# Kernel optimization log

Measured on AMD Instinct MI355X. Metric: run time of the kernel, lower is better.

Reference implementation:

```python
import jax, jax.numpy as jnp
import numpy as np

N_NODES = 50000
N_EDGES = 800000
F_IN = 128
F_OUT = 64
ALPHA = 0.2  # LeakyReLU negative slope


def setup_inputs() -> dict:
    key = jax.random.key(0)
    k1, k2, k3, k4, k5, k6 = jax.random.split(key, 6)
    inp = jax.random.normal(k1, (N_NODES, F_IN), dtype=jnp.float32)
    W = jax.random.normal(k2, (F_IN, F_OUT), dtype=jnp.float32) * 0.05
    a = jax.random.normal(k3, (1, 2 * F_OUT), dtype=jnp.float32) * 0.05
    adj_vals = jax.random.uniform(k4, (N_EDGES,), dtype=jnp.float32)
    src = jax.random.randint(k5, (N_EDGES,), 0, N_NODES)
    dst = jax.random.randint(k6, (N_EDGES,), 0, N_NODES)
    edge_index = jnp.stack([src, dst], axis=0).astype(jnp.int64)
    return {"input": inp, "W": W, "a": a, "adj_vals": adj_vals, "edge_index": edge_index}


def reference(input, W, a, adj_vals, edge_index):
    N = input.shape[0]
    src, dst = edge_index[0], edge_index[1]
    # h = input @ W  (dropout is identity in eval mode)
    h = input @ W  # (N, F_OUT)
    # a.mm(edge_h) with edge_h = [h[src]; h[dst]] decomposes into two per-node dots
    a_src, a_dst = a[0, :F_OUT], a[0, F_OUT:]
    score_src = h @ a_src  # (N,)
    score_dst = h @ a_dst  # (N,)
    scores = score_src[src] + score_dst[dst]  # (E,)
    edge_e = jnp.exp(-jax.nn.leaky_relu(scores, ALPHA)) * adj_vals  # (E,)
    # sparse spmm: row-sum normalizer and weighted aggregation over neighbors
    e_rowsum = jax.ops.segment_sum(edge_e, src, num_segments=N)  # (N,)
    h_prime = jax.ops.segment_sum(edge_e[:, None] * h[dst], src, num_segments=N)  # (N, F_OUT)
    h_prime = h_prime / e_rowsum[:, None]
    return jax.nn.elu(h_prime)  # concat=True
```

## Files before the change

### kernel.cpp

```cpp
#include <hip/hip_runtime.h>
#include <math.h>

#define N_NODES 50000
#define N_EDGES 800000
#define F_IN    128
#define F_OUT   64
#define ALPHA   0.2f

#define NP      50176
#define NB      196

__global__ __launch_bounds__(256) void k_gemm_scores(
    const float* __restrict__ in, const float* __restrict__ W,
    const float* __restrict__ a, float* __restrict__ h,
    float* __restrict__ ssrc, float* __restrict__ sdst) {
  __shared__ float Ws[F_IN][F_OUT];
  __shared__ float As[64][68];
  __shared__ float al[2 * F_OUT];

  const int tid  = threadIdx.x;
  const int row0 = blockIdx.x * 64;

  {
    const float4* Wg = reinterpret_cast<const float4*>(W);
    float4* Wl = reinterpret_cast<float4*>(&Ws[0][0]);
    #pragma unroll
    for (int i = 0; i < 8; ++i) Wl[tid + i * 256] = Wg[tid + i * 256];
  }
  if (tid < 2 * F_OUT) al[tid] = a[tid];

  const int rg = tid >> 4;
  const int cg = tid & 15;
  const int sr = tid >> 2;
  const int sq = tid & 3;
  int grow = row0 + sr; if (grow >= N_NODES) grow = N_NODES - 1;

  float acc[4][4] = {{0.f}};

  for (int kc = 0; kc < 2; ++kc) {
    if (kc) __syncthreads();
    #pragma unroll
    for (int i = 0; i < 4; ++i) {
      const int slot = sq + 4 * i;
      const float4 v = *reinterpret_cast<const float4*>(
          in + (size_t)grow * F_IN + kc * 64 + slot * 4);
      As[slot * 4 + 0][sr] = v.x;
      As[slot * 4 + 1][sr] = v.y;
      As[slot * 4 + 2][sr] = v.z;
      As[slot * 4 + 3][sr] = v.w;
    }
    __syncthreads();

    #pragma unroll 8
    for (int kk = 0; kk < 64; ++kk) {
      const float4 av = *reinterpret_cast<const float4*>(&As[kk][rg * 4]);
      const float4 bv = *reinterpret_cast<const float4*>(&Ws[kc * 64 + kk][cg * 4]);
      acc[0][0] = fmaf(av.x, bv.x, acc[0][0]);
      acc[0][1] = fmaf(av.x, bv.y, acc[0][1]);
      acc[0][2] = fmaf(av.x, bv.z, acc[0][2]);
      acc[0][3] = fmaf(av.x, bv.w, acc[0][3]);
      acc[1][0] = fmaf(av.y, bv.x, acc[1][0]);
      acc[1][1] = fmaf(av.y, bv.y, acc[1][1]);
      acc[1][2] = fmaf(av.y, bv.z, acc[1][2]);
      acc[1][3] = fmaf(av.y, bv.w, acc[1][3]);
      acc[2][0] = fmaf(av.z, bv.x, acc[2][0]);
      acc[2][1] = fmaf(av.z, bv.y, acc[2][1]);
      acc[2][2] = fmaf(av.z, bv.z, acc[2][2]);
      acc[2][3] = fmaf(av.z, bv.w, acc[2][3]);
      acc[3][0] = fmaf(av.w, bv.x, acc[3][0]);
      acc[3][1] = fmaf(av.w, bv.y, acc[3][1]);
      acc[3][2] = fmaf(av.w, bv.z, acc[3][2]);
      acc[3][3] = fmaf(av.w, bv.w, acc[3][3]);
    }
  }

  #pragma unroll
  for (int i = 0; i < 4; ++i) {
    const int row = row0 + rg * 4 + i;
    if (row < N_NODES) {
      float4 hv = make_float4(acc[i][0], acc[i][1], acc[i][2], acc[i][3]);
      *reinterpret_cast<float4*>(h + (size_t)row * F_OUT + cg * 4) = hv;
    }
  }

  float ssr[4], sdr[4];
  #pragma unroll
  for (int i = 0; i < 4; ++i) {
    ssr[i] = acc[i][0] * al[cg * 4 + 0] + acc[i][1] * al[cg * 4 + 1]
           + acc[i][2] * al[cg * 4 + 2] + acc[i][3] * al[cg * 4 + 3];
    sdr[i] = acc[i][0] * al[F_OUT + cg * 4 + 0] + acc[i][1] * al[F_OUT + cg * 4 + 1]
           + acc[i][2] * al[F_OUT + cg * 4 + 2] + acc[i][3] * al[F_OUT + cg * 4 + 3];
  }
  #pragma unroll
  for (int m = 1; m < 16; m <<= 1) {
    #pragma unroll
    for (int i = 0; i < 4; ++i) {
      ssr[i] += __shfl_xor(ssr[i], m);
      sdr[i] += __shfl_xor(sdr[i], m);
    }
  }
  if (cg == 0) {
    #pragma unroll
    for (int i = 0; i < 4; ++i) {
      const int row = row0 + rg * 4 + i;
      if (row < N_NODES) { ssrc[row] = ssr[i]; sdst[row] = sdr[i]; }
    }
  }
}

__global__ __launch_bounds__(256) void k_hist(const int* __restrict__ src,
                                              int* __restrict__ deg) {
  const int e = blockIdx.x * 256 + threadIdx.x;
  atomicAdd(&deg[src[e]], 1);
}

__global__ __launch_bounds__(256) void k_scan_a(const int* __restrict__ deg,
                                                int* __restrict__ offs,
                                                int* __restrict__ bsum) {
  __shared__ int lds[256];
  const int i = blockIdx.x * 256 + threadIdx.x;
  const int v = deg[i];
  lds[threadIdx.x] = v;
  __syncthreads();
  #pragma unroll
  for (int off = 1; off < 256; off <<= 1) {
    int t = (threadIdx.x >= off) ? lds[threadIdx.x - off] : 0;
    __syncthreads();
    lds[threadIdx.x] += t;
    __syncthreads();
  }
  offs[i] = lds[threadIdx.x] - v;
  if (threadIdx.x == 255) bsum[blockIdx.x] = lds[255];
}

__global__ __launch_bounds__(256) void k_scan_b(const int* __restrict__ bsum,
                                                int* __restrict__ boff) {
  __shared__ int lds[256];
  const int v = (threadIdx.x < NB) ? bsum[threadIdx.x] : 0;
  lds[threadIdx.x] = v;
  __syncthreads();
  #pragma unroll
  for (int off = 1; off < 256; off <<= 1) {
    int t = (threadIdx.x >= off) ? lds[threadIdx.x - off] : 0;
    __syncthreads();
    lds[threadIdx.x] += t;
    __syncthreads();
  }
  boff[threadIdx.x] = lds[threadIdx.x] - v;
}

__global__ __launch_bounds__(256) void k_scatter(
    const int* __restrict__ src, const int* __restrict__ dst,
    const float* __restrict__ adj,
    const float* __restrict__ ssrc, const float* __restrict__ sdst,
    const int* __restrict__ offs, const int* __restrict__ boff,
    int* __restrict__ cursor, int2* __restrict__ pairs) {
  const int e = blockIdx.x * 256 + threadIdx.x;
  const int s = src[e];
  const int d = dst[e];
  const float sc = ssrc[s] + sdst[d];
  const float lr = sc > 0.f ? sc : ALPHA * sc;
  const float ee = expf(-lr) * adj[e];
  const int base = offs[s] + boff[s >> 8];
  const int pos  = base + atomicAdd(&cursor[s], 1);
  pairs[pos] = make_int2(d, __float_as_int(ee));
}

__global__ __launch_bounds__(256) void k_gather(
    const int2* __restrict__ pairs, const int* __restrict__ offs,
    const int* __restrict__ boff, const float* __restrict__ h,
    float* __restrict__ out) {
  const int wave = threadIdx.x >> 6;
  const int lane = threadIdx.x & 63;
  const int node = blockIdx.x * 4 + wave;

  const int o0 = offs[node] + boff[node >> 8];
  const int o1 = offs[node + 1] + boff[(node + 1) >> 8];

  float acc = 0.f, rs = 0.f;
  int j = o0;
  for (; j + 3 < o1; j += 4) {
    const int2 p0 = pairs[j];
    const int2 p1 = pairs[j + 1];
    const int2 p2 = pairs[j + 2];
    const int2 p3 = pairs[j + 3];
    const float h0 = h[(size_t)p0.x * F_OUT + lane];
    const float h1 = h[(size_t)p1.x * F_OUT + lane];
    const float h2 = h[(size_t)p2.x * F_OUT + lane];
    const float h3 = h[(size_t)p3.x * F_OUT + lane];
    const float e0 = __int_as_float(p0.y);
    const float e1 = __int_as_float(p1.y);
    const float e2 = __int_as_float(p2.y);
    const float e3 = __int_as_float(p3.y);
    acc += e0 * h0; rs += e0;
    acc += e1 * h1; rs += e1;
    acc += e2 * h2; rs += e2;
    acc += e3 * h3; rs += e3;
  }
  for (; j < o1; ++j) {
    const int2 p = pairs[j];
    const float ee = __int_as_float(p.y);
    acc += ee * h[(size_t)p.x * F_OUT + lane];
    rs  += ee;
  }

  float v = acc / rs;
  v = v > 0.f ? v : expm1f(v);
  out[(size_t)node * F_OUT + lane] = v;
}

extern "C" void kernel_launch(void* const* d_in, const int* in_sizes, int n_in,
                              void* d_out, int out_size, void* d_ws, size_t ws_size,
                              hipStream_t stream) {
  const float* input = (const float*)d_in[0];
  const float* W     = (const float*)d_in[1];
  const float* a     = (const float*)d_in[2];
  const float* adj   = (const float*)d_in[3];
  const int*   ei    = (const int*)d_in[4];
  const int*   src   = ei;
  const int*   dst   = ei + N_EDGES;
  float* out = (float*)d_out;

  float* h    = (float*)d_ws;
  float* ssrc = h + (size_t)N_NODES * F_OUT;
  float* sdst = ssrc + N_NODES;
  int*   deg    = (int*)(sdst + N_NODES);
  int*   cursor = deg + NP;
  int*   offs   = cursor + NP;
  int*   bsum   = offs + NP;
  int*   boff   = bsum + 256;
  int2*  pairs  = (int2*)(boff + 256);

  hipMemsetAsync(deg, 0, 2 * NP * sizeof(int), stream);

  k_hist   <<<N_EDGES / 256, 256, 0, stream>>>(src, deg);
  k_scan_a <<<NB, 256, 0, stream>>>(deg, offs, bsum);
  k_scan_b <<<1, 256, 0, stream>>>(bsum, boff);
  k_gemm_scores<<<(N_NODES + 63) / 64, 256, 0, stream>>>(input, W, a, h, ssrc, sdst);
  k_scatter<<<N_EDGES / 256, 256, 0, stream>>>(src, dst, adj, ssrc, sdst,
                                               offs, boff, cursor, pairs);
  k_gather <<<N_NODES / 4, 256, 0, stream>>>(pairs, offs, boff, h, out);
}
```

Measured before the change: 216.3 us.

## Replace per-node CSR build with bucketed binning and LDS-local per-node sort

```diff
diff --git a/kernel.cpp b/kernel.cpp
--- a/kernel.cpp
+++ b/kernel.cpp
@@ -7,8 +7,10 @@
 #define F_OUT   64
 #define ALPHA   0.2f
 
-#define NP      50176
-#define NB      196
+#define NBKT    392
+#define BNODES  128
+#define EBLK    4096
+#define CHUNK   2048
 
 __global__ __launch_bounds__(256) void k_gemm_scores(
     const float* __restrict__ in, const float* __restrict__ W,
@@ -108,105 +110,168 @@
   }
 }
 
-__global__ __launch_bounds__(256) void k_hist(const int* __restrict__ src,
-                                              int* __restrict__ deg) {
+__global__ __launch_bounds__(256) void k_bhist(const int* __restrict__ src,
+                                               int* __restrict__ bcnt) {
+  __shared__ int lh[NBKT];
+  for (int i = threadIdx.x; i < NBKT; i += 256) lh[i] = 0;
+  __syncthreads();
   const int e = blockIdx.x * 256 + threadIdx.x;
-  atomicAdd(&deg[src[e]], 1);
-}
-
-__global__ __launch_bounds__(256) void k_scan_a(const int* __restrict__ deg,
-                                                int* __restrict__ offs,
-                                                int* __restrict__ bsum) {
-  __shared__ int lds[256];
-  const int i = blockIdx.x * 256 + threadIdx.x;
-  const int v = deg[i];
-  lds[threadIdx.x] = v;
-  __syncthreads();
-  #pragma unroll
-  for (int off = 1; off < 256; off <<= 1) {
-    int t = (threadIdx.x >= off) ? lds[threadIdx.x - off] : 0;
-    __syncthreads();
-    lds[threadIdx.x] += t;
-    __syncthreads();
-  }
-  offs[i] = lds[threadIdx.x] - v;
-  if (threadIdx.x == 255) bsum[blockIdx.x] = lds[255];
-}
-
-__global__ __launch_bounds__(256) void k_scan_b(const int* __restrict__ bsum,
-                                                int* __restrict__ boff) {
-  __shared__ int lds[256];
-  const int v = (threadIdx.x < NB) ? bsum[threadIdx.x] : 0;
-  lds[threadIdx.x] = v;
-  __syncthreads();
-  #pragma unroll
-  for (int off = 1; off < 256; off <<= 1) {
-    int t = (threadIdx.x >= off) ? lds[threadIdx.x - off] : 0;
-    __syncthreads();
-    lds[threadIdx.x] += t;
-    __syncthreads();
-  }
-  boff[threadIdx.x] = lds[threadIdx.x] - v;
-}
-
-__global__ __launch_bounds__(256) void k_scatter(
+  atomicAdd(&lh[src[e] >> 7], 1);
+  __syncthreads();
+  for (int i = threadIdx.x; i < NBKT; i += 256)
+    if (lh[i]) atomicAdd(&bcnt[i], lh[i]);
+}
+
+__global__ __launch_bounds__(512) void k_bscan(const int* __restrict__ bcnt,
+                                               int* __restrict__ bbase) {
+  __shared__ int scn[512];
+  const int tid = threadIdx.x;
+  const int v = (tid < NBKT) ? bcnt[tid] : 0;
+  scn[tid] = v;
+  __syncthreads();
+  #pragma unroll
+  for (int off = 1; off < 512; off <<= 1) {
+    int t = (tid >= off) ? scn[tid - off] : 0;
+    __syncthreads();
+    scn[tid] += t;
+    __syncthreads();
+  }
+  bbase[tid] = scn[tid] - v;
+}
+
+__global__ __launch_bounds__(512) void k_binscatter(
     const int* __restrict__ src, const int* __restrict__ dst,
     const float* __restrict__ adj,
     const float* __restrict__ ssrc, const float* __restrict__ sdst,
-    const int* __restrict__ offs, const int* __restrict__ boff,
-    int* __restrict__ cursor, int2* __restrict__ pairs) {
-  const int e = blockIdx.x * 256 + threadIdx.x;
-  const int s = src[e];
-  const int d = dst[e];
-  const float sc = ssrc[s] + sdst[d];
-  const float lr = sc > 0.f ? sc : ALPHA * sc;
-  const float ee = expf(-lr) * adj[e];
-  const int base = offs[s] + boff[s >> 8];
-  const int pos  = base + atomicAdd(&cursor[s], 1);
-  pairs[pos] = make_int2(d, __float_as_int(ee));
-}
-
-__global__ __launch_bounds__(256) void k_gather(
-    const int2* __restrict__ pairs, const int* __restrict__ offs,
-    const int* __restrict__ boff, const float* __restrict__ h,
-    float* __restrict__ out) {
-  const int wave = threadIdx.x >> 6;
-  const int lane = threadIdx.x & 63;
-  const int node = blockIdx.x * 4 + wave;
-
-  const int o0 = offs[node] + boff[node >> 8];
-  const int o1 = offs[node + 1] + boff[(node + 1) >> 8];
-
-  float acc = 0.f, rs = 0.f;
-  int j = o0;
-  for (; j + 3 < o1; j += 4) {
-    const int2 p0 = pairs[j];
-    const int2 p1 = pairs[j + 1];
-    const int2 p2 = pairs[j + 2];
-    const int2 p3 = pairs[j + 3];
-    const float h0 = h[(size_t)p0.x * F_OUT + lane];
-    const float h1 = h[(size_t)p1.x * F_OUT + lane];
-    const float h2 = h[(size_t)p2.x * F_OUT + lane];
-    const float h3 = h[(size_t)p3.x * F_OUT + lane];
-    const float e0 = __int_as_float(p0.y);
-    const float e1 = __int_as_float(p1.y);
-    const float e2 = __int_as_float(p2.y);
-    const float e3 = __int_as_float(p3.y);
-    acc += e0 * h0; rs += e0;
-    acc += e1 * h1; rs += e1;
-    acc += e2 * h2; rs += e2;
-    acc += e3 * h3; rs += e3;
-  }
-  for (; j < o1; ++j) {
-    const int2 p = pairs[j];
-    const float ee = __int_as_float(p.y);
-    acc += ee * h[(size_t)p.x * F_OUT + lane];
-    rs  += ee;
-  }
-
-  float v = acc / rs;
-  v = v > 0.f ? v : expm1f(v);
-  out[(size_t)node * F_OUT + lane] = v;
+    const int* __restrict__ bbase, int* __restrict__ bcursor,
+    int2* __restrict__ pairs) {
+  __shared__ int lh[512], lofs[512], lcur[512], gbase[512], scn[512];
+  __shared__ int2 led[EBLK];
+  const int tid = threadIdx.x;
+  const int e0  = blockIdx.x * EBLK;
+  const int cnt = min(EBLK, N_EDGES - e0);
+
+  lh[tid] = 0; lcur[tid] = 0;
+  __syncthreads();
+
+  int2 rec[8]; int rbkt[8];
+  #pragma unroll
+  for (int k = 0; k < 8; ++k) {
+    const int i = tid + k * 512;
+    rbkt[k] = -1;
+    if (i < cnt) {
+      const int e = e0 + i;
+      const int s = src[e], d = dst[e];
+      const float sc = ssrc[s] + sdst[d];
+      const float lr = sc > 0.f ? sc : ALPHA * sc;
+      const float ee = expf(-lr) * adj[e];
+      const int bkt = s >> 7;
+      const unsigned w0 = (unsigned)d | ((unsigned)(s & 127) << 16)
+                        | ((unsigned)bkt << 23);
+      rec[k]  = make_int2((int)w0, __float_as_int(ee));
+      rbkt[k] = bkt;
+      atomicAdd(&lh[bkt], 1);
+    }
+  }
+  __syncthreads();
+  scn[tid] = lh[tid];
+  __syncthreads();
+  #pragma unroll
+  for (int off = 1; off < 512; off <<= 1) {
+    int t = (tid >= off) ? scn[tid - off] : 0;
+    __syncthreads();
+    scn[tid] += t;
+    __syncthreads();
+  }
+  lofs[tid] = scn[tid] - lh[tid];
+  __syncthreads();
+  #pragma unroll
+  for (int k = 0; k < 8; ++k)
+    if (rbkt[k] >= 0)
+      led[lofs[rbkt[k]] + atomicAdd(&lcur[rbkt[k]], 1)] = rec[k];
+  if (tid < NBKT && lh[tid] > 0)
+    gbase[tid] = bbase[tid] + atomicAdd(&bcursor[tid], lh[tid]);
+  __syncthreads();
+  for (int i = tid; i < cnt; i += 512) {
+    const int2 r  = led[i];
+    const int bkt = ((unsigned)r.x) >> 23;
+    pairs[gbase[bkt] + (i - lofs[bkt])] = r;
+  }
+}
+
+__global__ __launch_bounds__(512) void k_gather_b(
+    const int2* __restrict__ pairs, const int* __restrict__ bbase,
+    const float* __restrict__ h, float* __restrict__ out) {
+  __shared__ int2 sed[CHUNK], sed2[CHUNK];
+  __shared__ int lh[BNODES], lofs[BNODES], lcur[BNODES], scn[BNODES];
+  const int tid  = threadIdx.x;
+  const int wav  = tid >> 6, lane = tid & 63;
+  const int b    = blockIdx.x;
+  const int e0   = bbase[b], e1 = bbase[b + 1];
+
+  float acc[16], rs[16];
+  #pragma unroll
+  for (int i = 0; i < 16; ++i) { acc[i] = 0.f; rs[i] = 0.f; }
+
+  for (int cs = e0; cs < e1; cs += CHUNK) {
+    const int cnt = min(CHUNK, e1 - cs);
+    __syncthreads();
+    if (tid < BNODES) { lh[tid] = 0; lcur[tid] = 0; }
+    __syncthreads();
+    for (int i = tid; i < cnt; i += 512) {
+      const int2 r = pairs[cs + i];
+      sed[i] = r;
+      atomicAdd(&lh[(r.x >> 16) & 127], 1);
+    }
+    __syncthreads();
+    if (tid < BNODES) scn[tid] = lh[tid];
+    __syncthreads();
+    #pragma unroll
+    for (int off = 1; off < BNODES; off <<= 1) {
+      int t = 0;
+      if (tid < BNODES && tid >= off) t = scn[tid - off];
+      __syncthreads();
+      if (tid < BNODES) scn[tid] += t;
+      __syncthreads();
+    }
+    if (tid < BNODES) lofs[tid] = scn[tid] - lh[tid];
+    __syncthreads();
+    for (int i = tid; i < cnt; i += 512) {
+      const int2 r = sed[i];
+      const int n  = (r.x >> 16) & 127;
+      sed2[lofs[n] + atomicAdd(&lcur[n], 1)] = r;
+    }
+    __syncthreads();
+    for (int i = 0; i < 16; ++i) {
+      const int nl = wav * 16 + i;
+      const int js = lofs[nl], je = js + lh[nl];
+      int j = js;
+      for (; j + 1 < je; j += 2) {
+        const int2 r0 = sed2[j], r1 = sed2[j + 1];
+        const float h0 = h[(size_t)(r0.x & 0xFFFF) * F_OUT + lane];
+        const float h1 = h[(size_t)(r1.x & 0xFFFF) * F_OUT + lane];
+        const float f0 = __int_as_float(r0.y), f1 = __int_as_float(r1.y);
+        acc[i] += f0 * h0; rs[i] += f0;
+        acc[i] += f1 * h1; rs[i] += f1;
+      }
+      if (j < je) {
+        const int2 r = sed2[j];
+        const float f = __int_as_float(r.y);
+        acc[i] += f * h[(size_t)(r.x & 0xFFFF) * F_OUT + lane];
+        rs[i]  += f;
+      }
+    }
+  }
+
+  #pragma unroll
+  for (int i = 0; i < 16; ++i) {
+    const int n = b * BNODES + wav * 16 + i;
+    if (n < N_NODES) {
+      float v = acc[i] / rs[i];
+      v = v > 0.f ? v : expm1f(v);
+      out[(size_t)n * F_OUT + lane] = v;
+    }
+  }
 }
 
 extern "C" void kernel_launch(void* const* d_in, const int* in_sizes, int n_in,
@@ -221,23 +286,20 @@
   const int*   dst   = ei + N_EDGES;
   float* out = (float*)d_out;
 
-  float* h    = (float*)d_ws;
-  float* ssrc = h + (size_t)N_NODES * F_OUT;
-  float* sdst = ssrc + N_NODES;
-  int*   deg    = (int*)(sdst + N_NODES);
-  int*   cursor = deg + NP;
-  int*   offs   = cursor + NP;
-  int*   bsum   = offs + NP;
-  int*   boff   = bsum + 256;
-  int2*  pairs  = (int2*)(boff + 256);
-
-  hipMemsetAsync(deg, 0, 2 * NP * sizeof(int), stream);
-
-  k_hist   <<<N_EDGES / 256, 256, 0, stream>>>(src, deg);
-  k_scan_a <<<NB, 256, 0, stream>>>(deg, offs, bsum);
-  k_scan_b <<<1, 256, 0, stream>>>(bsum, boff);
+  float* h      = (float*)d_ws;
+  float* ssrc   = h + (size_t)N_NODES * F_OUT;
+  float* sdst   = ssrc + N_NODES;
+  int*   bcnt    = (int*)(sdst + N_NODES);
+  int*   bcursor = bcnt + 512;
+  int*   bbase   = bcursor + 512;
+  int2*  pairs   = (int2*)(bbase + 512);
+
+  hipMemsetAsync(bcnt, 0, 1024 * sizeof(int), stream);
+
+  k_bhist      <<<N_EDGES / 256, 256, 0, stream>>>(src, bcnt);
+  k_bscan      <<<1, 512, 0, stream>>>(bcnt, bbase);
   k_gemm_scores<<<(N_NODES + 63) / 64, 256, 0, stream>>>(input, W, a, h, ssrc, sdst);
-  k_scatter<<<N_EDGES / 256, 256, 0, stream>>>(src, dst, adj, ssrc, sdst,
-                                               offs, boff, cursor, pairs);
-  k_gather <<<N_NODES / 4, 256, 0, stream>>>(pairs, offs, boff, h, out);
-}
+  k_binscatter <<<(N_EDGES + EBLK - 1) / EBLK, 512, 0, stream>>>(
+      src, dst, adj, ssrc, sdst, bbase, bcursor, pairs);
+  k_gather_b   <<<NBKT, 512, 0, stream>>>(pairs, bbase, h, out);
+}
```

Result: slower. 245.2 us (+13.4%).
